# Performance work log

Hardware: AMD Instinct MI355X
Metric: run time of the kernel (lower is better)

## Reference

```python
import jax, jax.numpy as jnp
import numpy as np

B, N, C = 4, 2048, 1024
H = 16
D = C // H  # head_dim = 64

def setup_inputs() -> dict:
    key = jax.random.key(0)
    k1, k2, k3 = jax.random.split(key, 3)
    s = 1.0 / np.sqrt(C)
    x = jax.random.normal(k1, (B, N, C), dtype=jnp.float32)
    qkv_w = jax.random.normal(k2, (3 * C, C), dtype=jnp.float32) * s
    proj_w = jax.random.normal(k3, (C, C), dtype=jnp.float32) * s
    proj_b = jnp.zeros((C,), dtype=jnp.float32)
    return {"x": x, "qkv_w": qkv_w, "proj_w": proj_w, "proj_b": proj_b}

def reference(x, qkv_w, proj_w, proj_b):
    # qkv: torch Linear -> x @ W^T, no bias
    qkv = jnp.einsum('bnc,oc->bno', x, qkv_w)            # [B,N,3C]
    qkv = qkv.reshape(B, N, 3, H, D)
    q, k, v = qkv[:, :, 0], qkv[:, :, 1], qkv[:, :, 2]   # [B,N,H,D]
    scale = D ** -0.5
    scores = jnp.einsum('bqhd,bkhd->bhqk', q, k) * scale  # [B,H,N,N]
    causal = jnp.tril(jnp.ones((N, N), dtype=bool))
    scores = jnp.where(causal[None, None], scores, -jnp.inf)
    attn = jax.nn.softmax(scores, axis=-1)
    out = jnp.einsum('bhqk,bkhd->bqhd', attn, v).reshape(B, N, C)
    out = jnp.einsum('bnc,oc->bno', out, proj_w) + proj_b
    return out
```

## Files before the change

kernel.cpp:

```cpp
#include <hip/hip_runtime.h>
#include <math.h>

typedef __attribute__((ext_vector_type(8))) short short8;
typedef __attribute__((ext_vector_type(4))) short short4v;
typedef __attribute__((ext_vector_type(4))) float f32x4;
typedef __attribute__((ext_vector_type(4))) _Float16 half4v;

#define B_  4
#define N_  2048
#define C_  1024
#define H_  16
#define D_  64
#define TC3 3072

__device__ __forceinline__ short f2bf(float f) {
    unsigned u = __builtin_bit_cast(unsigned, f);
    u += 0x7fffu + ((u >> 16) & 1u);
    return (short)(u >> 16);
}

__device__ __forceinline__ half4v pack4h(float a, float b, float cc, float d) {
    auto lo = __builtin_amdgcn_cvt_pkrtz(a, b);
    auto hi = __builtin_amdgcn_cvt_pkrtz(cc, d);
    auto v4 = __builtin_shufflevector(lo, hi, 0, 1, 2, 3);
    return __builtin_bit_cast(half4v, v4);
}

__device__ __forceinline__ void gload16(const void* g, void* l) {
    __builtin_amdgcn_global_load_lds(
        (const __attribute__((address_space(1))) void*)g,
        (__attribute__((address_space(3))) void*)l, 16, 0, 0);
}

#define NX8  (B_ * N_ * C_ / 8)
#define NQ8  (TC3 * C_ / 8)
#define NP8  (C_ * C_ / 8)

__global__ __launch_bounds__(256) void cast_all(const float* __restrict__ x,
                                                const float* __restrict__ wq,
                                                const float* __restrict__ wp,
                                                short* __restrict__ xb,
                                                short* __restrict__ wqb,
                                                short* __restrict__ wpb) {
    int i = blockIdx.x * 256 + threadIdx.x;
    const float* src;
    short* dst;
    if (i < NX8) { src = x; dst = xb; }
    else if (i < NX8 + NQ8) { i -= NX8; src = wq; dst = wqb; }
    else { i -= NX8 + NQ8; src = wp; dst = wpb; }
    const float4 a = ((const float4*)src)[2 * i];
    const float4 b = ((const float4*)src)[2 * i + 1];
    short8 t;
    t[0] = f2bf(a.x); t[1] = f2bf(a.y); t[2] = f2bf(a.z); t[3] = f2bf(a.w);
    t[4] = f2bf(b.x); t[5] = f2bf(b.y); t[6] = f2bf(b.z); t[7] = f2bf(b.w);
    ((short8*)dst)[i] = t;
}

#define GK 64

template <int MODE>
__global__ __launch_bounds__(256) void gemm_bf16(const short* __restrict__ A,
                                                 const short* __restrict__ Bw,
                                                 const float* __restrict__ bias,
                                                 short* __restrict__ Qb,
                                                 short* __restrict__ Kb,
                                                 _Float16* __restrict__ Vtb,
                                                 float* __restrict__ Fout,
                                                 int M, int Nn, int K) {
    __shared__ short smem[2 * 128 * GK];
    short* As = smem;
    short* Bs = smem + 128 * GK;

    const int tid = threadIdx.x;
    const int w = tid >> 6;
    const int ln = tid & 63;
    const int wm = w >> 1;
    const int wn = w & 1;
    const int c = ln & 15;
    const int g = ln >> 4;
    const int c7 = c & 7;

    const int m0 = blockIdx.y * 128;
    const int n0 = blockIdx.x * 128;

    f32x4 acc[4][4];
#pragma unroll
    for (int m = 0; m < 4; ++m)
#pragma unroll
        for (int n = 0; n < 4; ++n) acc[m][n] = (f32x4){0.f, 0.f, 0.f, 0.f};

    const int srow = ln >> 3;
    const int sseg = (ln & 7) ^ srow;

    for (int k0 = 0; k0 < K; k0 += GK) {
#pragma unroll
        for (int j = 0; j < 4; ++j) {
            const int R0 = w * 32 + j * 8;
            const int row = R0 + srow;
            gload16(A + (size_t)(m0 + row) * K + k0 + sseg * 8, &As[R0 * GK]);
            gload16(Bw + (size_t)(n0 + row) * K + k0 + sseg * 8, &Bs[R0 * GK]);
        }
        asm volatile("s_waitcnt vmcnt(0)" ::: "memory");
        __syncthreads();

#pragma unroll
        for (int kh = 0; kh < 2; ++kh) {
            short8 aF[4], bF[4];
#pragma unroll
            for (int m = 0; m < 4; ++m)
                aF[m] = *(const short8*)&As[(wm * 64 + m * 16 + c) * GK +
                                            (((kh * 4 + g) ^ c7) * 8)];
#pragma unroll
            for (int n = 0; n < 4; ++n)
                bF[n] = *(const short8*)&Bs[(wn * 64 + n * 16 + c) * GK +
                                            (((kh * 4 + g) ^ c7) * 8)];
#pragma unroll
            for (int m = 0; m < 4; ++m)
#pragma unroll
                for (int n = 0; n < 4; ++n)
                    acc[m][n] = __builtin_amdgcn_mfma_f32_16x16x32_bf16(aF[m], bF[n], acc[m][n], 0, 0, 0);
        }
        __syncthreads();
    }

    if (MODE == 0) {
        const int mat = n0 >> 10;
        if (mat == 2) {
#pragma unroll
            for (int m = 0; m < 4; ++m) {
                const int row = m0 + wm * 64 + m * 16 + g * 4;
                const int b = row >> 11;
                const int nseq = row & 2047;
#pragma unroll
                for (int n = 0; n < 4; ++n) {
                    const int col = n0 + wn * 64 + n * 16 + c;
                    const int h = (col >> 6) & 15;
                    const int d = col & 63;
                    const half4v p = pack4h(acc[m][n][0], acc[m][n][1],
                                            acc[m][n][2], acc[m][n][3]);
                    *(half4v*)&Vtb[((size_t)(b * 16 + h) * 64 + d) * N_ + nseq] = p;
                }
            }
        } else {
            short* base = (mat == 0) ? Qb : Kb;
#pragma unroll
            for (int p = 0; p < 2; ++p) {
                __syncthreads();
                if (wn == p) {
#pragma unroll
                    for (int m = 0; m < 4; ++m)
#pragma unroll
                        for (int n = 0; n < 4; ++n)
#pragma unroll
                            for (int r = 0; r < 4; ++r)
                                smem[(wm * 64 + m * 16 + g * 4 + r) * 64 +
                                     (((n ^ g) * 16) + c)] = f2bf(acc[m][n][r]);
                }
                __syncthreads();
                const int row = tid >> 1;
                const int col0 = (tid & 1) * 32;
                const int gg = (row >> 2) & 3;
                const int grow = m0 + row;
                const int bb = grow >> 11, nseq = grow & 2047;
                const int h = ((n0 + p * 64) >> 6) & 15;
                short* dst = base + ((size_t)(bb * 16 + h) * N_ + nseq) * D_ + col0;
#pragma unroll
                for (int s16 = 0; s16 < 2; ++s16) {
                    const int Cb = col0 + s16 * 16;
                    const int ls_off = row * 64 + ((((Cb >> 4) ^ gg)) << 4);
                    *(short8*)(dst + s16 * 16) = *(const short8*)&smem[ls_off];
                    *(short8*)(dst + s16 * 16 + 8) = *(const short8*)&smem[ls_off + 8];
                }
            }
        }
    } else {
#pragma unroll
        for (int m = 0; m < 4; ++m) {
            const int row = m0 + wm * 64 + m * 16 + g * 4;
#pragma unroll
            for (int n = 0; n < 4; ++n) {
                const int col = n0 + wn * 64 + n * 16 + c;
                const float bv = bias[col];
#pragma unroll
                for (int r = 0; r < 4; ++r)
                    Fout[(size_t)(row + r) * Nn + col] = acc[m][n][r] + bv;
            }
        }
    }
}


__constant__ unsigned char CH_QT[40] = {0,1,2,3, 4,4, 5,5, 6,6, 7,7,
                                        8,8,8, 9,9,9, 10,10,10, 11,11,11,
                                        12,12,12,12, 13,13,13,13, 14,14,14,14, 15,15,15,15};
__constant__ unsigned char CH_C0[40] = {0,0,0,0, 0,1, 0,1, 0,1, 0,1,
                                        0,1,2, 0,1,2, 0,1,2, 0,1,2,
                                        0,1,2,3, 0,1,2,3, 0,1,2,3, 0,1,2,3};
__constant__ unsigned char CH_BASE[16] = {0,1,2,3,4,6,8,10,12,15,18,21,24,28,32,36};

__device__ __forceinline__ void stage_kv(const short* __restrict__ gK,
                                         const short* __restrict__ gV,
                                         short* KsB, short* VsB,
                                         int kt, int w, int lane) {
    const int sub = lane >> 3;
    const int sseg = (lane & 7) ^ sub;
#pragma unroll
    for (int j = 0; j < 2; ++j) {
        const int R0 = w * 16 + j * 8;
        const int row = R0 + sub;
        gload16(gK + (size_t)(kt * 64 + row) * D_ + sseg * 8, KsB + R0 * 64);
        gload16(gV + (size_t)row * N_ + kt * 64 + sseg * 8, VsB + R0 * 64);
    }
}

__global__ __launch_bounds__(256, 4) void attn_part(const short* __restrict__ Qb,
                                                    const short* __restrict__ Kb,
                                                    const _Float16* __restrict__ Vtb,
                                                    _Float16* __restrict__ Pp,
                                                    float* __restrict__ Lp) {
    __shared__ short Ks[2][64 * 64];
    __shared__ short Vts[2][64 * 64];

    const int bh = blockIdx.y;
    const int f = blockIdx.x;
    const int qt = CH_QT[f];
    const int kt0 = CH_C0[f] * 8;
    const int kt1 = min(kt0 + 8, 2 * qt + 2);

    const int tid = threadIdx.x;
    const int w = tid >> 6;
    const int lane = tid & 63;
    const int g = lane >> 4;
    const int c = lane & 15;
    const int swz = c & 7;
    const int rowmin = qt * 128 + w * 32;

    const short* gK = Kb + (size_t)bh * N_ * D_;
    const short* gV = (const short*)(Vtb + (size_t)bh * D_ * N_);

    short8 aQ[2][2];
    {
        const short* qb0 = Qb + ((size_t)bh * N_ + rowmin) * D_;
#pragma unroll
        for (int m = 0; m < 2; ++m) {
            aQ[m][0] = *(const short8*)(qb0 + (m * 16 + c) * D_ + g * 8);
            aQ[m][1] = *(const short8*)(qb0 + (m * 16 + c) * D_ + 32 + g * 8);
        }
    }

    f32x4 Oacc[2][4];
#pragma unroll
    for (int m = 0; m < 2; ++m)
#pragma unroll
        for (int nt = 0; nt < 4; ++nt) Oacc[m][nt] = (f32x4){0.f, 0.f, 0.f, 0.f};
    float ls[2] = {0.f, 0.f};

    stage_kv(gK, gV, Ks[0], Vts[0], kt0, w, lane);

    for (int kt = kt0; kt < kt1; ++kt) {
        const short* KsB = Ks[kt & 1];
        const short* VsB = Vts[kt & 1];
        asm volatile("s_waitcnt vmcnt(0)" ::: "memory");
        __syncthreads();
        if (kt + 1 < kt1)
            stage_kv(gK, gV, Ks[(kt + 1) & 1], Vts[(kt + 1) & 1], kt + 1, w, lane);

        const int kvb = kt * 64;
        if (kvb > rowmin + 31) continue;
        const bool needmask = (kvb + 63) > rowmin;

        f32x4 S[2][4];
#pragma unroll
        for (int m = 0; m < 2; ++m)
#pragma unroll
            for (int n = 0; n < 4; ++n) S[m][n] = (f32x4){0.f, 0.f, 0.f, 0.f};
#pragma unroll
        for (int n = 0; n < 4; ++n) {
            const short* kr = KsB + (n * 16 + c) * 64;
            const short8 bk0 = *(const short8*)(kr + (g ^ swz) * 8);
            const short8 bk1 = *(const short8*)(kr + ((4 + g) ^ swz) * 8);
#pragma unroll
            for (int m = 0; m < 2; ++m) {
                S[m][n] = __builtin_amdgcn_mfma_f32_16x16x32_bf16(bk0, aQ[m][0], S[m][n], 0, 0, 0);
                S[m][n] = __builtin_amdgcn_mfma_f32_16x16x32_bf16(bk1, aQ[m][1], S[m][n], 0, 0, 0);
            }
        }

        half4v Pb[2][4];
#pragma unroll
        for (int m = 0; m < 2; ++m) {
            const int qrow = rowmin + m * 16 + c;
#pragma unroll
            for (int n = 0; n < 4; ++n) {
                float p[4];
#pragma unroll
                for (int r = 0; r < 4; ++r) {
                    float pv = __expf(fmaf(S[m][n][r], 0.125f, -4.0f));
                    if (needmask && (kvb + n * 16 + g * 4 + r) > qrow) pv = 0.f;
                    ls[m] += pv;
                    p[r] = pv;
                }
                Pb[m][n] = pack4h(p[0], p[1], p[2], p[3]);
            }
        }

#pragma unroll
        for (int n = 0; n < 4; ++n) {
#pragma unroll
            for (int nt = 0; nt < 4; ++nt) {
                const int vrow = nt * 16 + c;
                const int vseg = (n * 2 + (g >> 1)) ^ swz;
                const half4v av = *(const half4v*)&VsB[vrow * 64 + vseg * 8 + (g & 1) * 4];
#pragma unroll
                for (int m = 0; m < 2; ++m)
                    Oacc[m][nt] = __builtin_amdgcn_mfma_f32_16x16x16f16(av, Pb[m][n], Oacc[m][nt], 0, 0, 0);
            }
        }
    }

#pragma unroll
    for (int m = 0; m < 2; ++m) {
        ls[m] += __shfl_xor(ls[m], 16);
        ls[m] += __shfl_xor(ls[m], 32);
    }

    const size_t slot = (size_t)bh * 40 + f;
    _Float16* dst = Pp + slot * (128 * 64);
#pragma unroll
    for (int m = 0; m < 2; ++m) {
        const int q = w * 32 + m * 16 + c;
#pragma unroll
        for (int nt = 0; nt < 4; ++nt) {
            const half4v o = pack4h(Oacc[m][nt][0], Oacc[m][nt][1],
                                    Oacc[m][nt][2], Oacc[m][nt][3]);
            *(half4v*)&dst[q * 64 + nt * 16 + g * 4] = o;
        }
        if (g == 0) Lp[slot * 128 + q] = ls[m];
    }
}

__global__ __launch_bounds__(256) void attn_reduce(const _Float16* __restrict__ Pp,
                                                   const float* __restrict__ Lp,
                                                   short* __restrict__ attnb) {
    const int qt = blockIdx.x;
    const int bh = blockIdx.y;
    const int b = bh >> 4, h = bh & 15;
    const int nc = (2 * qt + 2 + 7) / 8;
    const size_t slot0 = (size_t)bh * 40 + CH_BASE[qt];

    const int tid = threadIdx.x;
    const int q = tid >> 1;
    const int dh = (tid & 1) * 32;

    float acc[32];
#pragma unroll
    for (int i = 0; i < 32; ++i) acc[i] = 0.f;
    float l = 0.f;

    for (int cix = 0; cix < nc; ++cix) {
        const size_t s = slot0 + cix;
        l += Lp[s * 128 + q];
        const _Float16* p = Pp + s * (128 * 64) + q * 64 + dh;
#pragma unroll
        for (int v = 0; v < 4; ++v) {
            const half4v h4a = *(const half4v*)(p + v * 8);
            const half4v h4b = *(const half4v*)(p + v * 8 + 4);
#pragma unroll
            for (int r = 0; r < 4; ++r) {
                acc[v * 8 + r] += (float)h4a[r];
                acc[v * 8 + 4 + r] += (float)h4b[r];
            }
        }
    }

    const float inv = 1.0f / l;
    short* dst = attnb + (size_t)(b * N_ + qt * 128 + q) * C_ + h * D_ + dh;
#pragma unroll
    for (int v = 0; v < 4; ++v) {
        short8 o;
#pragma unroll
        for (int r = 0; r < 8; ++r) o[r] = f2bf(acc[v * 8 + r] * inv);
        *(short8*)(dst + v * 8) = o;
    }
}

extern "C" void kernel_launch(void* const* d_in, const int* in_sizes, int n_in,
                              void* d_out, int out_size, void* d_ws, size_t ws_size,
                              hipStream_t stream) {
    const float* x      = (const float*)d_in[0];
    const float* qkv_w  = (const float*)d_in[1];
    const float* proj_w = (const float*)d_in[2];
    const float* proj_b = (const float*)d_in[3];
    float* out = (float*)d_out;

    short* xb      = (short*)d_ws;
    short* qkv_wb  = xb + (size_t)B_ * N_ * C_;
    short* proj_wb = qkv_wb + (size_t)TC3 * C_;
    short* Qb      = proj_wb + (size_t)C_ * C_;
    short* Kb      = Qb + (size_t)B_ * H_ * N_ * D_;
    _Float16* Vtb  = (_Float16*)(Kb + (size_t)B_ * H_ * N_ * D_);
    short* attnb   = (short*)(Vtb + (size_t)B_ * H_ * N_ * D_);
    _Float16* Pp   = (_Float16*)(attnb + (size_t)B_ * N_ * C_);
    float* Lp      = (float*)(Pp + (size_t)64 * 40 * 128 * 64);

    const int M = B_ * N_;
    dim3 blk(256);

    cast_all<<<dim3((NX8 + NQ8 + NP8) / 256), blk, 0, stream>>>(
        x, qkv_w, proj_w, xb, qkv_wb, proj_wb);

    gemm_bf16<0><<<dim3(TC3 / 128, M / 128), blk, 0, stream>>>(
        xb, qkv_wb, nullptr, Qb, Kb, Vtb, nullptr, M, TC3, C_);

    attn_part<<<dim3(40, B_ * H_), blk, 0, stream>>>(Qb, Kb, Vtb, Pp, Lp);
    attn_reduce<<<dim3(N_ / 128, B_ * H_), blk, 0, stream>>>(Pp, Lp, attnb);

    gemm_bf16<1><<<dim3(C_ / 128, M / 128), blk, 0, stream>>>(
        attnb, proj_wb, proj_b, nullptr, nullptr, nullptr, out, M, C_, C_);
}
```

Before: 272.1 us.

## Replace split-KV attention and reduce with persistent atomic-queue fused attention

```diff
diff --git a/kernel.cpp b/kernel.cpp
--- a/kernel.cpp
+++ b/kernel.cpp
@@ -190,14 +190,6 @@
 }
 
 
-__constant__ unsigned char CH_QT[40] = {0,1,2,3, 4,4, 5,5, 6,6, 7,7,
-                                        8,8,8, 9,9,9, 10,10,10, 11,11,11,
-                                        12,12,12,12, 13,13,13,13, 14,14,14,14, 15,15,15,15};
-__constant__ unsigned char CH_C0[40] = {0,0,0,0, 0,1, 0,1, 0,1, 0,1,
-                                        0,1,2, 0,1,2, 0,1,2, 0,1,2,
-                                        0,1,2,3, 0,1,2,3, 0,1,2,3, 0,1,2,3};
-__constant__ unsigned char CH_BASE[16] = {0,1,2,3,4,6,8,10,12,15,18,21,24,28,32,36};
-
 __device__ __forceinline__ void stage_kv(const short* __restrict__ gK,
                                          const short* __restrict__ gV,
                                          short* KsB, short* VsB,
@@ -213,19 +205,16 @@
     }
 }
 
-__global__ __launch_bounds__(256, 4) void attn_part(const short* __restrict__ Qb,
-                                                    const short* __restrict__ Kb,
-                                                    const _Float16* __restrict__ Vtb,
-                                                    _Float16* __restrict__ Pp,
-                                                    float* __restrict__ Lp) {
+#define NITEMS 1024
+
+__global__ __launch_bounds__(256, 4) void attn_fused(const short* __restrict__ Qb,
+                                                     const short* __restrict__ Kb,
+                                                     const _Float16* __restrict__ Vtb,
+                                                     short* __restrict__ attnb,
+                                                     unsigned int* __restrict__ counter) {
     __shared__ short Ks[2][64 * 64];
     __shared__ short Vts[2][64 * 64];
-
-    const int bh = blockIdx.y;
-    const int f = blockIdx.x;
-    const int qt = CH_QT[f];
-    const int kt0 = CH_C0[f] * 8;
-    const int kt1 = min(kt0 + 8, 2 * qt + 2);
+    __shared__ int s_item;
 
     const int tid = threadIdx.x;
     const int w = tid >> 6;
@@ -233,154 +222,121 @@
     const int g = lane >> 4;
     const int c = lane & 15;
     const int swz = c & 7;
-    const int rowmin = qt * 128 + w * 32;
-
-    const short* gK = Kb + (size_t)bh * N_ * D_;
-    const short* gV = (const short*)(Vtb + (size_t)bh * D_ * N_);
-
-    short8 aQ[2][2];
-    {
-        const short* qb0 = Qb + ((size_t)bh * N_ + rowmin) * D_;
+
+    for (;;) {
+        __syncthreads();
+        if (tid == 0) s_item = (int)atomicAdd(counter, 1u);
+        __syncthreads();
+        const int idx = s_item;
+        if (idx >= NITEMS) return;
+
+        const int qt = 15 - (idx >> 6);
+        const int bh = idx & 63;
+        const int b = bh >> 4, h = bh & 15;
+        const int rowmin = qt * 128 + w * 32;
+        const int nkt = 2 * qt + 2;
+
+        const short* gK = Kb + (size_t)bh * N_ * D_;
+        const short* gV = (const short*)(Vtb + (size_t)bh * D_ * N_);
+
+        short8 aQ[2][2];
+        {
+            const short* qb0 = Qb + ((size_t)bh * N_ + rowmin) * D_;
+#pragma unroll
+            for (int m = 0; m < 2; ++m) {
+                aQ[m][0] = *(const short8*)(qb0 + (m * 16 + c) * D_ + g * 8);
+                aQ[m][1] = *(const short8*)(qb0 + (m * 16 + c) * D_ + 32 + g * 8);
+            }
+        }
+
+        f32x4 Oacc[2][4];
+#pragma unroll
+        for (int m = 0; m < 2; ++m)
+#pragma unroll
+            for (int nt = 0; nt < 4; ++nt) Oacc[m][nt] = (f32x4){0.f, 0.f, 0.f, 0.f};
+        float ls[2] = {0.f, 0.f};
+
+        stage_kv(gK, gV, Ks[0], Vts[0], 0, w, lane);
+
+        for (int kt = 0; kt < nkt; ++kt) {
+            const short* KsB = Ks[kt & 1];
+            const short* VsB = Vts[kt & 1];
+            asm volatile("s_waitcnt vmcnt(0)" ::: "memory");
+            __syncthreads();
+            if (kt + 1 < nkt)
+                stage_kv(gK, gV, Ks[(kt + 1) & 1], Vts[(kt + 1) & 1], kt + 1, w, lane);
+
+            const int kvb = kt * 64;
+            if (kvb > rowmin + 31) continue;
+            const bool needmask = (kvb + 63) > rowmin;
+
+            f32x4 S[2][4];
+#pragma unroll
+            for (int m = 0; m < 2; ++m)
+#pragma unroll
+                for (int n = 0; n < 4; ++n) S[m][n] = (f32x4){0.f, 0.f, 0.f, 0.f};
+#pragma unroll
+            for (int n = 0; n < 4; ++n) {
+                const short* kr = KsB + (n * 16 + c) * 64;
+                const short8 bk0 = *(const short8*)(kr + (g ^ swz) * 8);
+                const short8 bk1 = *(const short8*)(kr + ((4 + g) ^ swz) * 8);
+#pragma unroll
+                for (int m = 0; m < 2; ++m) {
+                    S[m][n] = __builtin_amdgcn_mfma_f32_16x16x32_bf16(bk0, aQ[m][0], S[m][n], 0, 0, 0);
+                    S[m][n] = __builtin_amdgcn_mfma_f32_16x16x32_bf16(bk1, aQ[m][1], S[m][n], 0, 0, 0);
+                }
+            }
+
+            half4v Pb[2][4];
+#pragma unroll
+            for (int m = 0; m < 2; ++m) {
+                const int qrow = rowmin + m * 16 + c;
+#pragma unroll
+                for (int n = 0; n < 4; ++n) {
+                    float p[4];
+#pragma unroll
+                    for (int r = 0; r < 4; ++r) {
+                        float pv = __expf(fmaf(S[m][n][r], 0.125f, -4.0f));
+                        if (needmask && (kvb + n * 16 + g * 4 + r) > qrow) pv = 0.f;
+                        ls[m] += pv;
+                        p[r] = pv;
+                    }
+                    Pb[m][n] = pack4h(p[0], p[1], p[2], p[3]);
+                }
+            }
+
+#pragma unroll
+            for (int n = 0; n < 4; ++n) {
+#pragma unroll
+                for (int nt = 0; nt < 4; ++nt) {
+                    const int vrow = nt * 16 + c;
+                    const int vseg = (n * 2 + (g >> 1)) ^ swz;
+                    const half4v av = *(const half4v*)&VsB[vrow * 64 + vseg * 8 + (g & 1) * 4];
+#pragma unroll
+                    for (int m = 0; m < 2; ++m)
+                        Oacc[m][nt] = __builtin_amdgcn_mfma_f32_16x16x16f16(av, Pb[m][n], Oacc[m][nt], 0, 0, 0);
+                }
+            }
+        }
+
 #pragma unroll
         for (int m = 0; m < 2; ++m) {
-            aQ[m][0] = *(const short8*)(qb0 + (m * 16 + c) * D_ + g * 8);
-            aQ[m][1] = *(const short8*)(qb0 + (m * 16 + c) * D_ + 32 + g * 8);
-        }
-    }
-
-    f32x4 Oacc[2][4];
-#pragma unroll
-    for (int m = 0; m < 2; ++m)
-#pragma unroll
-        for (int nt = 0; nt < 4; ++nt) Oacc[m][nt] = (f32x4){0.f, 0.f, 0.f, 0.f};
-    float ls[2] = {0.f, 0.f};
-
-    stage_kv(gK, gV, Ks[0], Vts[0], kt0, w, lane);
-
-    for (int kt = kt0; kt < kt1; ++kt) {
-        const short* KsB = Ks[kt & 1];
-        const short* VsB = Vts[kt & 1];
-        asm volatile("s_waitcnt vmcnt(0)" ::: "memory");
-        __syncthreads();
-        if (kt + 1 < kt1)
-            stage_kv(gK, gV, Ks[(kt + 1) & 1], Vts[(kt + 1) & 1], kt + 1, w, lane);
-
-        const int kvb = kt * 64;
-        if (kvb > rowmin + 31) continue;
-        const bool needmask = (kvb + 63) > rowmin;
-
-        f32x4 S[2][4];
-#pragma unroll
-        for (int m = 0; m < 2; ++m)
-#pragma unroll
-            for (int n = 0; n < 4; ++n) S[m][n] = (f32x4){0.f, 0.f, 0.f, 0.f};
-#pragma unroll
-        for (int n = 0; n < 4; ++n) {
-            const short* kr = KsB + (n * 16 + c) * 64;
-            const short8 bk0 = *(const short8*)(kr + (g ^ swz) * 8);
-            const short8 bk1 = *(const short8*)(kr + ((4 + g) ^ swz) * 8);
-#pragma unroll
-            for (int m = 0; m < 2; ++m) {
-                S[m][n] = __builtin_amdgcn_mfma_f32_16x16x32_bf16(bk0, aQ[m][0], S[m][n], 0, 0, 0);
-                S[m][n] = __builtin_amdgcn_mfma_f32_16x16x32_bf16(bk1, aQ[m][1], S[m][n], 0, 0, 0);
-            }
-        }
-
-        half4v Pb[2][4];
+            ls[m] += __shfl_xor(ls[m], 16);
+            ls[m] += __shfl_xor(ls[m], 32);
+        }
 #pragma unroll
         for (int m = 0; m < 2; ++m) {
+            const float inv = 1.0f / ls[m];
             const int qrow = rowmin + m * 16 + c;
-#pragma unroll
-            for (int n = 0; n < 4; ++n) {
-                float p[4];
-#pragma unroll
-                for (int r = 0; r < 4; ++r) {
-                    float pv = __expf(fmaf(S[m][n][r], 0.125f, -4.0f));
-                    if (needmask && (kvb + n * 16 + g * 4 + r) > qrow) pv = 0.f;
-                    ls[m] += pv;
-                    p[r] = pv;
-                }
-                Pb[m][n] = pack4h(p[0], p[1], p[2], p[3]);
-            }
-        }
-
-#pragma unroll
-        for (int n = 0; n < 4; ++n) {
+            short* dst = attnb + (size_t)(b * N_ + qrow) * C_ + h * D_;
 #pragma unroll
             for (int nt = 0; nt < 4; ++nt) {
-                const int vrow = nt * 16 + c;
-                const int vseg = (n * 2 + (g >> 1)) ^ swz;
-                const half4v av = *(const half4v*)&VsB[vrow * 64 + vseg * 8 + (g & 1) * 4];
-#pragma unroll
-                for (int m = 0; m < 2; ++m)
-                    Oacc[m][nt] = __builtin_amdgcn_mfma_f32_16x16x16f16(av, Pb[m][n], Oacc[m][nt], 0, 0, 0);
-            }
-        }
-    }
-
-#pragma unroll
-    for (int m = 0; m < 2; ++m) {
-        ls[m] += __shfl_xor(ls[m], 16);
-        ls[m] += __shfl_xor(ls[m], 32);
-    }
-
-    const size_t slot = (size_t)bh * 40 + f;
-    _Float16* dst = Pp + slot * (128 * 64);
-#pragma unroll
-    for (int m = 0; m < 2; ++m) {
-        const int q = w * 32 + m * 16 + c;
-#pragma unroll
-        for (int nt = 0; nt < 4; ++nt) {
-            const half4v o = pack4h(Oacc[m][nt][0], Oacc[m][nt][1],
-                                    Oacc[m][nt][2], Oacc[m][nt][3]);
-            *(half4v*)&dst[q * 64 + nt * 16 + g * 4] = o;
-        }
-        if (g == 0) Lp[slot * 128 + q] = ls[m];
-    }
-}
-
-__global__ __launch_bounds__(256) void attn_reduce(const _Float16* __restrict__ Pp,
-                                                   const float* __restrict__ Lp,
-                                                   short* __restrict__ attnb) {
-    const int qt = blockIdx.x;
-    const int bh = blockIdx.y;
-    const int b = bh >> 4, h = bh & 15;
-    const int nc = (2 * qt + 2 + 7) / 8;
-    const size_t slot0 = (size_t)bh * 40 + CH_BASE[qt];
-
-    const int tid = threadIdx.x;
-    const int q = tid >> 1;
-    const int dh = (tid & 1) * 32;
-
-    float acc[32];
-#pragma unroll
-    for (int i = 0; i < 32; ++i) acc[i] = 0.f;
-    float l = 0.f;
-
-    for (int cix = 0; cix < nc; ++cix) {
-        const size_t s = slot0 + cix;
-        l += Lp[s * 128 + q];
-        const _Float16* p = Pp + s * (128 * 64) + q * 64 + dh;
-#pragma unroll
-        for (int v = 0; v < 4; ++v) {
-            const half4v h4a = *(const half4v*)(p + v * 8);
-            const half4v h4b = *(const half4v*)(p + v * 8 + 4);
-#pragma unroll
-            for (int r = 0; r < 4; ++r) {
-                acc[v * 8 + r] += (float)h4a[r];
-                acc[v * 8 + 4 + r] += (float)h4b[r];
-            }
-        }
-    }
-
-    const float inv = 1.0f / l;
-    short* dst = attnb + (size_t)(b * N_ + qt * 128 + q) * C_ + h * D_ + dh;
-#pragma unroll
-    for (int v = 0; v < 4; ++v) {
-        short8 o;
-#pragma unroll
-        for (int r = 0; r < 8; ++r) o[r] = f2bf(acc[v * 8 + r] * inv);
-        *(short8*)(dst + v * 8) = o;
+                short4v o;
+#pragma unroll
+                for (int r = 0; r < 4; ++r) o[r] = f2bf(Oacc[m][nt][r] * inv);
+                *(short4v*)(dst + nt * 16 + g * 4) = o;
+            }
+        }
     }
 }
 
@@ -400,20 +356,20 @@
     short* Kb      = Qb + (size_t)B_ * H_ * N_ * D_;
     _Float16* Vtb  = (_Float16*)(Kb + (size_t)B_ * H_ * N_ * D_);
     short* attnb   = (short*)(Vtb + (size_t)B_ * H_ * N_ * D_);
-    _Float16* Pp   = (_Float16*)(attnb + (size_t)B_ * N_ * C_);
-    float* Lp      = (float*)(Pp + (size_t)64 * 40 * 128 * 64);
+    unsigned int* cnt = (unsigned int*)(attnb + (size_t)B_ * N_ * C_);
 
     const int M = B_ * N_;
     dim3 blk(256);
 
+    hipMemsetAsync(cnt, 0, sizeof(unsigned int), stream);
+
     cast_all<<<dim3((NX8 + NQ8 + NP8) / 256), blk, 0, stream>>>(
         x, qkv_w, proj_w, xb, qkv_wb, proj_wb);
 
     gemm_bf16<0><<<dim3(TC3 / 128, M / 128), blk, 0, stream>>>(
         xb, qkv_wb, nullptr, Qb, Kb, Vtb, nullptr, M, TC3, C_);
 
-    attn_part<<<dim3(40, B_ * H_), blk, 0, stream>>>(Qb, Kb, Vtb, Pp, Lp);
-    attn_reduce<<<dim3(N_ / 128, B_ * H_), blk, 0, stream>>>(Pp, Lp, attnb);
+    attn_fused<<<dim3(768), blk, 0, stream>>>(Qb, Kb, Vtb, attnb, cnt);
 
     gemm_bf16<1><<<dim3(C_ / 128, M / 128), blk, 0, stream>>>(
         attnb, proj_wb, proj_b, nullptr, nullptr, nullptr, out, M, C_, C_);
```

After: 261.5 us. 1.04x faster.
